# Kernel tuning notes

Measured on AMD Instinct MI355X. Metric: run time of the kernel, lower is better.

## Reference

```python
import jax, jax.numpy as jnp
import numpy as np

IN_CH = 256
OUT_CH = 512
K = 4        # kernel_size (== input spatial size)
STRIDE = 1
PADDING = 0
GROUPS = 1
B = 32


def setup_inputs() -> dict:
    key = jax.random.key(0)
    ks = jax.random.split(key, 7)
    x = jax.random.normal(ks[0], (B, IN_CH, K, K), dtype=jnp.float32)
    s1 = 1.0 / np.sqrt(IN_CH)
    W1 = jax.random.normal(ks[1], (IN_CH, IN_CH), dtype=jnp.float32) * s1
    b1 = jax.random.normal(ks[2], (IN_CH,), dtype=jnp.float32) * s1
    W2 = jax.random.normal(ks[3], (OUT_CH * IN_CH, IN_CH), dtype=jnp.float32) * s1
    b2 = jax.random.normal(ks[4], (OUT_CH * IN_CH,), dtype=jnp.float32) * s1
    Wa = jax.random.normal(ks[5], (OUT_CH * IN_CH, IN_CH), dtype=jnp.float32) * s1
    ba = jax.random.normal(ks[6], (OUT_CH * IN_CH,), dtype=jnp.float32) * s1
    return {"x": x, "W1": W1, "b1": b1, "W2": W2, "b2": b2, "Wa": Wa, "ba": ba}


def _conv1x1(x, W, b):
    # x: [b, cin, h, w], W: [cout, cin], b: [cout]
    return jnp.einsum('bchw,oc->bohw', x, W) + b[None, :, None, None]


def reference(x, W1, b1, W2, b2, Wa, ba):
    b, c, h, w = x.shape  # h == w == K
    # AvgPool2d(K): non-overlapping K x K mean pooling -> [b, c, 1, 1] here
    avg = x.reshape(b, c, h // K, K, w // K, K).mean(axis=(3, 5))
    # attention branch (computed but unused downstream, as in original)
    att = jax.nn.sigmoid(_conv1x1(avg, Wa, ba))
    att = att.reshape(-1, IN_CH, K, K)
    # dynamic per-sample weights
    weight = jax.nn.relu(_conv1x1(x, W1, b1))
    weight = _conv1x1(weight, W2, b2)            # [b, OUT_CH*IN_CH, K, K]
    weight = weight.reshape(-1, IN_CH, K, K)     # [b*OUT_CH, IN_CH, K, K]
    # batch-as-groups grouped conv
    xg = x.reshape(1, b * c, h, w)
    out = jax.lax.conv_general_dilated(
        xg, weight,
        window_strides=(STRIDE, STRIDE),
        padding=[(PADDING, PADDING), (PADDING, PADDING)],
        dimension_numbers=('NCHW', 'OIHW', 'NCHW'),
        feature_group_count=GROUPS * b,
    )  # [1, b*OUT_CH, oh, ow]
    return out.reshape(b, OUT_CH, out.shape[-2], out.shape[-1])
```

## Files before the change

### kernel.cpp

```cpp
#include <hip/hip_runtime.h>

#define IC 256
#define OC 512
#define NB 32
#define NP 16
#define KTOT 65536
#define NKC 64
#define KCH 1024
#define KS2 64

__global__ void kA(const float* __restrict__ x, const float* __restrict__ W1,
                   const float* __restrict__ b1, float* __restrict__ h) {
    int bp = blockIdx.x;
    int b = bp >> 4, p = bp & 15;
    int c = threadIdx.x;
    __shared__ float xs[IC];
    xs[c] = x[b * 4096 + c * 16 + p];
    __syncthreads();
    float acc = b1[c];
    const float* wrow = W1 + c * IC;
    #pragma unroll 8
    for (int i = 0; i < IC; i += 4) {
        float4 w = *(const float4*)(wrow + i);
        acc += w.x * xs[i] + w.y * xs[i + 1] + w.z * xs[i + 2] + w.w * xs[i + 3];
    }
    h[b * 4096 + c * 16 + p] = fmaxf(acc, 0.f);
}

__global__ void kB(const float* __restrict__ x, const float* __restrict__ h,
                   float* __restrict__ Gt, float* __restrict__ sx) {
    int i = blockIdx.x;
    int c = threadIdx.x;
    __shared__ float xsh[NB * NP];
    for (int e = c; e < NB * NP; e += 256) {
        int b = e >> 4, p = e & 15;
        xsh[e] = x[b * 4096 + i * 16 + p];
    }
    __syncthreads();
    float g[NB];
    const float* hbase = h + c * 16;
    #pragma unroll 8
    for (int b = 0; b < NB; ++b) {
        float4 x0 = *(const float4*)&xsh[b * 16];
        float4 x1 = *(const float4*)&xsh[b * 16 + 4];
        float4 x2 = *(const float4*)&xsh[b * 16 + 8];
        float4 x3 = *(const float4*)&xsh[b * 16 + 12];
        const float* hp = hbase + b * 4096;
        float4 h0 = *(const float4*)(hp);
        float4 h1 = *(const float4*)(hp + 4);
        float4 h2 = *(const float4*)(hp + 8);
        float4 h3 = *(const float4*)(hp + 12);
        g[b] = x0.x * h0.x + x0.y * h0.y + x0.z * h0.z + x0.w * h0.w
             + x1.x * h1.x + x1.y * h1.y + x1.z * h1.z + x1.w * h1.w
             + x2.x * h2.x + x2.y * h2.y + x2.z * h2.z + x2.w * h2.w
             + x3.x * h3.x + x3.y * h3.y + x3.z * h3.z + x3.w * h3.w;
    }
    float* gout = Gt + (size_t)i * 8192 + (size_t)c * 32;
    #pragma unroll
    for (int j = 0; j < 8; ++j) {
        float4 v = make_float4(g[j * 4], g[j * 4 + 1], g[j * 4 + 2], g[j * 4 + 3]);
        *(float4*)(gout + j * 4) = v;
    }
    if (c < NB) {
        float s = 0.f;
        #pragma unroll
        for (int p = 0; p < 16; ++p) s += xsh[c * 16 + p];
        sx[c * IC + i] = s;
    }
}

__global__ void kC(const float* __restrict__ W2, const float* __restrict__ Gt,
                   float* __restrict__ partial) {
    __shared__ float w2s[KS2 * 65];
    __shared__ float gs[KS2 * 32];
    int tid = threadIdx.x;
    int kc = blockIdx.x;
    int o0 = blockIdx.y * 64;
    int k0 = kc * KCH;
    int bg = tid >> 5;
    int ov = tid & 31;
    int so = tid >> 4;
    int su = tid & 15;

    float acc[4][2];
    #pragma unroll
    for (int ii = 0; ii < 4; ++ii) { acc[ii][0] = 0.f; acc[ii][1] = 0.f; }

    for (int ks = 0; ks < KCH; ks += KS2) {
        __syncthreads();
        #pragma unroll
        for (int pass = 0; pass < 4; ++pass) {
            int o_l = so + pass * 16;
            float4 v = *(const float4*)(W2 + (size_t)(o0 + o_l) * KTOT + (k0 + ks + su * 4));
            float* dst = &w2s[o_l * 65 + su * 4];
            dst[0] = v.x; dst[1] = v.y; dst[2] = v.z; dst[3] = v.w;
        }
        #pragma unroll
        for (int pass = 0; pass < 2; ++pass) {
            int f = tid + pass * 256;
            *(float4*)&gs[f * 4] = *(const float4*)(Gt + (size_t)(k0 + ks) * 32 + f * 4);
        }
        __syncthreads();
        #pragma unroll 4
        for (int k = 0; k < KS2; ++k) {
            float4 g = *(float4*)&gs[k * 32 + bg * 4];
            float w0 = w2s[(ov * 2) * 65 + k];
            float w1 = w2s[(ov * 2 + 1) * 65 + k];
            acc[0][0] += g.x * w0; acc[0][1] += g.x * w1;
            acc[1][0] += g.y * w0; acc[1][1] += g.y * w1;
            acc[2][0] += g.z * w0; acc[2][1] += g.z * w1;
            acc[3][0] += g.w * w0; acc[3][1] += g.w * w1;
        }
    }
    float* pout = partial + (size_t)kc * 16384 + o0 + ov * 2;
    #pragma unroll
    for (int ii = 0; ii < 4; ++ii) {
        int b = bg * 4 + ii;
        *(float2*)(pout + b * 512) = make_float2(acc[ii][0], acc[ii][1]);
    }
}

__global__ void kBias(const float* __restrict__ b2, const float* __restrict__ sx,
                      float* __restrict__ bias) {
    __shared__ float sxs[32 * 260];
    __shared__ float b2s[8 * 260];
    int tid = threadIdx.x;
    int o0 = blockIdx.x * 8;
    #pragma unroll
    for (int p = 0; p < 32; ++p) {
        int f = tid + p * 256;
        sxs[(f >> 8) * 260 + (f & 255)] = sx[f];
    }
    #pragma unroll
    for (int p = 0; p < 8; ++p) {
        int f = tid + p * 256;
        b2s[(f >> 8) * 260 + (f & 255)] = b2[(size_t)o0 * 256 + f];
    }
    __syncthreads();
    int b = tid >> 3, ol = tid & 7;
    float acc = 0.f;
    #pragma unroll 8
    for (int i = 0; i < 256; i += 4) {
        float4 sv = *(float4*)&sxs[b * 260 + i];
        float4 wv = *(float4*)&b2s[ol * 260 + i];
        acc += sv.x * wv.x + sv.y * wv.y + sv.z * wv.z + sv.w * wv.w;
    }
    bias[b * 512 + o0 + ol] = acc;
}

__global__ void kRed(const float* __restrict__ partial, const float* __restrict__ bias,
                     float* __restrict__ out) {
    __shared__ float red[256];
    int tid = threadIdx.x;
    int q = tid >> 6, jj = tid & 63;
    int j = blockIdx.x * 64 + jj;
    float s = 0.f;
    #pragma unroll
    for (int t = 0; t < 16; ++t)
        s += partial[(size_t)(q * 16 + t) * 16384 + j];
    red[tid] = s;
    __syncthreads();
    if (tid < 64)
        out[j] = red[jj] + red[64 + jj] + red[128 + jj] + red[192 + jj] + bias[j];
}

extern "C" void kernel_launch(void* const* d_in, const int* in_sizes, int n_in,
                              void* d_out, int out_size, void* d_ws, size_t ws_size,
                              hipStream_t stream) {
    const float* x  = (const float*)d_in[0];
    const float* W1 = (const float*)d_in[1];
    const float* b1 = (const float*)d_in[2];
    const float* W2 = (const float*)d_in[3];
    const float* b2 = (const float*)d_in[4];
    float* out = (float*)d_out;
    float* ws = (float*)d_ws;

    float* h       = ws;
    float* sx      = ws + 131072;
    float* Gt      = ws + 139264;
    float* partial = ws + 2236416;
    float* bias    = ws;

    kA<<<NB * NP, 256, 0, stream>>>(x, W1, b1, h);
    kB<<<IC, 256, 0, stream>>>(x, h, Gt, sx);
    kBias<<<64, 256, 0, stream>>>(b2, sx, bias);
    kC<<<dim3(NKC, 8), 256, 0, stream>>>(W2, Gt, partial);
    kRed<<<256, 256, 0, stream>>>(partial, bias, out);
}
```

Before: 319.3 us.

## Register-tile W2 GEMM with 8x8 outputs per thread and split-K over all outputs

Replaces the W2 contraction kernel with one where each block covers all 512 outputs and all 32 batches over a K-chunk. Each thread holds an 8x8 accumulator tile and reads W2 rows directly from global memory into registers, with the G operand staged transposed in shared memory. The G intermediate is rebuilt by a new kernel in batch-major layout, and the number of K-chunks (128 or 512) is picked from the workspace size, which the reduction kernel now takes as a parameter. The aim is to raise arithmetic intensity and make the 128 MB W2 stream bandwidth-bound. The cost is much higher register pressure and a larger partial-sum buffer to reduce.

```diff
diff --git a/kernel.cpp b/kernel.cpp
--- a/kernel.cpp
+++ b/kernel.cpp
@@ -5,9 +5,7 @@
 #define NB 32
 #define NP 16
 #define KTOT 65536
-#define NKC 64
-#define KCH 1024
-#define KS2 64
+#define KSUB 128
 
 __global__ void kA(const float* __restrict__ x, const float* __restrict__ W1,
                    const float* __restrict__ b1, float* __restrict__ h) {
@@ -27,96 +25,117 @@
     h[b * 4096 + c * 16 + p] = fmaxf(acc, 0.f);
 }
 
-__global__ void kB(const float* __restrict__ x, const float* __restrict__ h,
-                   float* __restrict__ Gt, float* __restrict__ sx) {
-    int i = blockIdx.x;
-    int c = threadIdx.x;
-    __shared__ float xsh[NB * NP];
-    for (int e = c; e < NB * NP; e += 256) {
-        int b = e >> 4, p = e & 15;
-        xsh[e] = x[b * 4096 + i * 16 + p];
-    }
-    __syncthreads();
-    float g[NB];
-    const float* hbase = h + c * 16;
-    #pragma unroll 8
-    for (int b = 0; b < NB; ++b) {
-        float4 x0 = *(const float4*)&xsh[b * 16];
-        float4 x1 = *(const float4*)&xsh[b * 16 + 4];
-        float4 x2 = *(const float4*)&xsh[b * 16 + 8];
-        float4 x3 = *(const float4*)&xsh[b * 16 + 12];
-        const float* hp = hbase + b * 4096;
-        float4 h0 = *(const float4*)(hp);
-        float4 h1 = *(const float4*)(hp + 4);
-        float4 h2 = *(const float4*)(hp + 8);
-        float4 h3 = *(const float4*)(hp + 12);
-        g[b] = x0.x * h0.x + x0.y * h0.y + x0.z * h0.z + x0.w * h0.w
-             + x1.x * h1.x + x1.y * h1.y + x1.z * h1.z + x1.w * h1.w
-             + x2.x * h2.x + x2.y * h2.y + x2.z * h2.z + x2.w * h2.w
-             + x3.x * h3.x + x3.y * h3.y + x3.z * h3.z + x3.w * h3.w;
-    }
-    float* gout = Gt + (size_t)i * 8192 + (size_t)c * 32;
-    #pragma unroll
-    for (int j = 0; j < 8; ++j) {
-        float4 v = make_float4(g[j * 4], g[j * 4 + 1], g[j * 4 + 2], g[j * 4 + 3]);
-        *(float4*)(gout + j * 4) = v;
-    }
-    if (c < NB) {
+__global__ void kB2(const float* __restrict__ x, const float* __restrict__ h,
+                    float* __restrict__ G2, float* __restrict__ sx) {
+    int bid = blockIdx.x;
+    int b = bid >> 3, it = (bid >> 1) & 3, ct = bid & 1;
+    __shared__ float xT[16 * 64];
+    __shared__ float hs[128 * 16];
+    int tid = threadIdx.x;
+    {
+        int il = tid >> 2, pq = tid & 3;
+        float4 v = *(const float4*)(x + b * 4096 + (it * 64 + il) * 16 + pq * 4);
+        xT[(pq * 4 + 0) * 64 + il] = v.x;
+        xT[(pq * 4 + 1) * 64 + il] = v.y;
+        xT[(pq * 4 + 2) * 64 + il] = v.z;
+        xT[(pq * 4 + 3) * 64 + il] = v.w;
+    }
+    #pragma unroll
+    for (int r = 0; r < 2; ++r) {
+        int idx = r * 1024 + tid * 4;
+        *(float4*)&hs[idx] = *(const float4*)(h + b * 4096 + ct * 2048 + idx);
+    }
+    __syncthreads();
+    int w = tid >> 6;
+    int il = tid & 63;
+    float xr[16];
+    #pragma unroll
+    for (int p = 0; p < 16; ++p) xr[p] = xT[p * 64 + il];
+    float* gbase = G2 + (size_t)b * KTOT + (size_t)(it * 64 + il) * 256 + ct * 128 + w * 32;
+    #pragma unroll
+    for (int c4 = 0; c4 < 8; ++c4) {
+        float g4[4];
+        #pragma unroll
+        for (int cc = 0; cc < 4; ++cc) {
+            int cl = w * 32 + c4 * 4 + cc;
+            const float* hp = &hs[cl * 16];
+            float4 h0 = *(const float4*)(hp);
+            float4 h1 = *(const float4*)(hp + 4);
+            float4 h2 = *(const float4*)(hp + 8);
+            float4 h3 = *(const float4*)(hp + 12);
+            g4[cc] = xr[0] * h0.x + xr[1] * h0.y + xr[2] * h0.z + xr[3] * h0.w
+                   + xr[4] * h1.x + xr[5] * h1.y + xr[6] * h1.z + xr[7] * h1.w
+                   + xr[8] * h2.x + xr[9] * h2.y + xr[10] * h2.z + xr[11] * h2.w
+                   + xr[12] * h3.x + xr[13] * h3.y + xr[14] * h3.z + xr[15] * h3.w;
+        }
+        *(float4*)(gbase + c4 * 4) = make_float4(g4[0], g4[1], g4[2], g4[3]);
+    }
+    if (ct == 0 && tid < 64) {
         float s = 0.f;
         #pragma unroll
-        for (int p = 0; p < 16; ++p) s += xsh[c * 16 + p];
-        sx[c * IC + i] = s;
-    }
-}
-
-__global__ void kC(const float* __restrict__ W2, const float* __restrict__ Gt,
-                   float* __restrict__ partial) {
-    __shared__ float w2s[KS2 * 65];
-    __shared__ float gs[KS2 * 32];
-    int tid = threadIdx.x;
-    int kc = blockIdx.x;
-    int o0 = blockIdx.y * 64;
-    int k0 = kc * KCH;
-    int bg = tid >> 5;
-    int ov = tid & 31;
-    int so = tid >> 4;
-    int su = tid & 15;
-
-    float acc[4][2];
-    #pragma unroll
-    for (int ii = 0; ii < 4; ++ii) { acc[ii][0] = 0.f; acc[ii][1] = 0.f; }
-
-    for (int ks = 0; ks < KCH; ks += KS2) {
+        for (int p = 0; p < 16; ++p) s += xr[p];
+        sx[b * 256 + it * 64 + tid] = s;
+    }
+}
+
+__global__ __launch_bounds__(256, 2) void kC3(const float* __restrict__ W2,
+        const float* __restrict__ G2, float* __restrict__ partial, int kchunk) {
+    __shared__ float gs[KSUB * 32];
+    int tid = threadIdx.x;
+    int tb = tid & 3;
+    int to = tid >> 2;
+    int k0 = blockIdx.x * kchunk;
+    float acc[8][8];
+    #pragma unroll
+    for (int ii = 0; ii < 8; ++ii)
+        #pragma unroll
+        for (int jj = 0; jj < 8; ++jj) acc[ii][jj] = 0.f;
+    const float* wbase = W2 + (size_t)(to * 8) * KTOT + k0;
+
+    for (int kc = 0; kc < kchunk; kc += KSUB) {
         __syncthreads();
-        #pragma unroll
-        for (int pass = 0; pass < 4; ++pass) {
-            int o_l = so + pass * 16;
-            float4 v = *(const float4*)(W2 + (size_t)(o0 + o_l) * KTOT + (k0 + ks + su * 4));
-            float* dst = &w2s[o_l * 65 + su * 4];
-            dst[0] = v.x; dst[1] = v.y; dst[2] = v.z; dst[3] = v.w;
-        }
-        #pragma unroll
-        for (int pass = 0; pass < 2; ++pass) {
-            int f = tid + pass * 256;
-            *(float4*)&gs[f * 4] = *(const float4*)(Gt + (size_t)(k0 + ks) * 32 + f * 4);
+        {
+            int sb = tid >> 3, q = tid & 7;
+            const float* gsrc = G2 + (size_t)sb * KTOT + k0 + kc;
+            #pragma unroll
+            for (int pp = 0; pp < 4; ++pp) {
+                int quad = q + pp * 8;
+                float4 v = *(const float4*)(gsrc + quad * 4);
+                int kl = quad * 4;
+                gs[(kl + 0) * 32 + sb] = v.x;
+                gs[(kl + 1) * 32 + sb] = v.y;
+                gs[(kl + 2) * 32 + sb] = v.z;
+                gs[(kl + 3) * 32 + sb] = v.w;
+            }
         }
         __syncthreads();
-        #pragma unroll 4
-        for (int k = 0; k < KS2; ++k) {
-            float4 g = *(float4*)&gs[k * 32 + bg * 4];
-            float w0 = w2s[(ov * 2) * 65 + k];
-            float w1 = w2s[(ov * 2 + 1) * 65 + k];
-            acc[0][0] += g.x * w0; acc[0][1] += g.x * w1;
-            acc[1][0] += g.y * w0; acc[1][1] += g.y * w1;
-            acc[2][0] += g.z * w0; acc[2][1] += g.z * w1;
-            acc[3][0] += g.w * w0; acc[3][1] += g.w * w1;
+        for (int ks = 0; ks < KSUB; ks += 8) {
+            float wv[8][8];
+            #pragma unroll
+            for (int jj = 0; jj < 8; ++jj) {
+                const float* wp = wbase + (size_t)jj * KTOT + kc + ks;
+                *(float4*)&wv[jj][0] = *(const float4*)(wp);
+                *(float4*)&wv[jj][4] = *(const float4*)(wp + 4);
+            }
+            #pragma unroll
+            for (int kk = 0; kk < 8; ++kk) {
+                float g8[8];
+                *(float4*)&g8[0] = *(float4*)&gs[(ks + kk) * 32 + tb * 8];
+                *(float4*)&g8[4] = *(float4*)&gs[(ks + kk) * 32 + tb * 8 + 4];
+                #pragma unroll
+                for (int ii = 0; ii < 8; ++ii)
+                    #pragma unroll
+                    for (int jj = 0; jj < 8; ++jj)
+                        acc[ii][jj] += g8[ii] * wv[jj][kk];
+            }
         }
     }
-    float* pout = partial + (size_t)kc * 16384 + o0 + ov * 2;
-    #pragma unroll
-    for (int ii = 0; ii < 4; ++ii) {
-        int b = bg * 4 + ii;
-        *(float2*)(pout + b * 512) = make_float2(acc[ii][0], acc[ii][1]);
+    float* pout = partial + (size_t)blockIdx.x * 16384;
+    #pragma unroll
+    for (int ii = 0; ii < 8; ++ii) {
+        int b = tb * 8 + ii;
+        *(float4*)(pout + b * 512 + to * 8)     = make_float4(acc[ii][0], acc[ii][1], acc[ii][2], acc[ii][3]);
+        *(float4*)(pout + b * 512 + to * 8 + 4) = make_float4(acc[ii][4], acc[ii][5], acc[ii][6], acc[ii][7]);
     }
 }
 
@@ -149,15 +168,15 @@
 }
 
 __global__ void kRed(const float* __restrict__ partial, const float* __restrict__ bias,
-                     float* __restrict__ out) {
+                     float* __restrict__ out, int nkc) {
     __shared__ float red[256];
     int tid = threadIdx.x;
     int q = tid >> 6, jj = tid & 63;
     int j = blockIdx.x * 64 + jj;
+    int per = nkc >> 2;
     float s = 0.f;
-    #pragma unroll
-    for (int t = 0; t < 16; ++t)
-        s += partial[(size_t)(q * 16 + t) * 16384 + j];
+    for (int t = 0; t < per; ++t)
+        s += partial[(size_t)(q * per + t) * 16384 + j];
     red[tid] = s;
     __syncthreads();
     if (tid < 64)
@@ -177,13 +196,17 @@
 
     float* h       = ws;
     float* sx      = ws + 131072;
-    float* Gt      = ws + 139264;
+    float* G2      = ws + 139264;
     float* partial = ws + 2236416;
     float* bias    = ws;
 
+    size_t avail = (ws_size / 4 > 2236416) ? ws_size / 4 - 2236416 : 0;
+    int nkc = (avail >= (size_t)512 * 16384) ? 512 : 128;
+    int kchunk = KTOT / nkc;
+
     kA<<<NB * NP, 256, 0, stream>>>(x, W1, b1, h);
-    kB<<<IC, 256, 0, stream>>>(x, h, Gt, sx);
+    kB2<<<256, 256, 0, stream>>>(x, h, G2, sx);
     kBias<<<64, 256, 0, stream>>>(b2, sx, bias);
-    kC<<<dim3(NKC, 8), 256, 0, stream>>>(W2, Gt, partial);
-    kRed<<<256, 256, 0, stream>>>(partial, bias, out);
-}
+    kC3<<<nkc, 256, 0, stream>>>(W2, G2, partial, kchunk);
+    kRed<<<256, 256, 0, stream>>>(partial, bias, out, nkc);
+}
```

Result: slower. 422.2 us (+32.2%).
